# Performance work log

Measured on AMD Instinct MI355X. Metric: run time of the kernel, lower is better.

Reference implementation:

```python
import jax, jax.numpy as jnp
import numpy as np

MERSENNE_P = (1 << 31) - 1  # prime used by universal hashing


def _uhash_cols(random_numbers, n_full_cols, n_comp_cols):
    """Universal-hash map from full-weight column index -> compressed column index.
    h(j) = ((r0*j + r1) mod P) mod n_comp_cols  (ints stay well within int64).
    """
    j = jnp.arange(n_full_cols, dtype=jnp.int64)
    r0 = random_numbers[0]
    r1 = random_numbers[1]
    return ((r0 * j + r1) % MERSENNE_P) % n_comp_cols


def setup_inputs() -> dict:
    key = jax.random.key(0)
    k1, k2, k3 = jax.random.split(key, 3)
    in_features, out_features, redn_factor = 8192, 8192, 4
    init_scale = 1.0 / np.sqrt(in_features)
    x = jax.random.normal(k1, (64, in_features), dtype=jnp.float32)
    weight = jax.random.uniform(
        k2, (out_features, in_features // redn_factor), dtype=jnp.float32,
        minval=-init_scale, maxval=init_scale)
    random_numbers = jax.random.randint(k3, (4,), 1, 1048576, dtype=jnp.int64)
    return {"x": x, "weight": weight, "random_numbers": random_numbers,
            "redn_factor": 4}


def reference(x, weight, random_numbers, redn_factor):
    # x: [..., K]; weight (compressed): [N, K // redn_factor]
    orig_shape = x.shape
    K = orig_shape[-1]
    x2d = x.reshape(-1, K)                      # preprocess: flatten leading dims
    n_comp = weight.shape[1]
    col_idx = _uhash_cols(random_numbers, K, n_comp)   # [K] hashed gather indices
    w_full = weight[:, col_idx]                 # [N, K] expanded via hashed gather
    y = x2d @ w_full.T                          # [rows, N]
    return y.reshape(*orig_shape[:-1], y.shape[-1])  # postprocess
```

## Files before the change

### kernel.cpp

```cpp
#include <hip/hip_runtime.h>
#include <hip/hip_bf16.h>

#define K_FULL   8192
#define M_ROWS   64
#define N_OUT    8192
#define N_COMP   2048
#define P_MERS   2147483647


typedef __attribute__((ext_vector_type(8))) short bf16x8;
typedef __attribute__((ext_vector_type(4))) float f32x4;

__device__ __forceinline__ short f2bfs(float f) {
    __hip_bfloat16 h = __float2bfloat16(f);
    return *reinterpret_cast<short*>(&h);
}
__device__ __forceinline__ unsigned int pk2bf(float a, float b) {
    return (unsigned int)(unsigned short)f2bfs(a)
         | ((unsigned int)(unsigned short)f2bfs(b) << 16);
}

#define GLL(g, l) __builtin_amdgcn_global_load_lds(                          \
    (const __attribute__((address_space(1))) unsigned int*)(g),             \
    (__attribute__((address_space(3))) unsigned int*)(l), 16, 0, 0)

__device__ __forceinline__ int hash_col(int j, int rn0, int rn1, int rn2, int rn3) {
    if (rn1 == 0 && rn3 == 0) {
        unsigned long long xx = (unsigned long long)(unsigned int)rn0 * (unsigned int)j
                              + (unsigned long long)(unsigned int)rn2;
        unsigned long long t = (xx & (unsigned long long)P_MERS) + (xx >> 31);
        if (t >= (unsigned long long)P_MERS) t -= (unsigned long long)P_MERS;
        return (int)(t & (N_COMP - 1));
    } else {
        unsigned int t = (unsigned int)rn0 * (unsigned int)j + (unsigned int)rn1;
        int ti = (int)t;
        int m1 = ti % P_MERS;
        if (m1 < 0) m1 += P_MERS;
        return m1 & (N_COMP - 1);
    }
}

__global__ __launch_bounds__(1024) void k_xc(const float* __restrict__ x,
                                             const int* __restrict__ rn,
                                             unsigned int* __restrict__ xcF) {
    __shared__ float row[N_COMP];
    const int m = blockIdx.x;
    const int tid = threadIdx.x;
    row[tid] = 0.0f;
    row[tid + 1024] = 0.0f;
    const int rn0 = rn[0], rn1 = rn[1], rn2 = rn[2], rn3 = rn[3];
    __syncthreads();

    const float* xm = x + (size_t)m * K_FULL;
#pragma unroll
    for (int it = 0; it < 2; ++it) {
        int j0 = tid * 4 + it * 4096;
        float4 v = *(const float4*)(xm + j0);
        atomicAdd(&row[hash_col(j0 + 0, rn0, rn1, rn2, rn3)], v.x);
        atomicAdd(&row[hash_col(j0 + 1, rn0, rn1, rn2, rn3)], v.y);
        atomicAdd(&row[hash_col(j0 + 2, rn0, rn1, rn2, rn3)], v.z);
        atomicAdd(&row[hash_col(j0 + 3, rn0, rn1, rn2, rn3)], v.w);
    }
    __syncthreads();

    const int c0 = 2 * tid;
    const int s  = c0 >> 5;
    const int kg = (c0 >> 3) & 3;
    const int e0 = c0 & 7;
    const int g  = m >> 4;
    const int nr = m & 15;
    xcF[(((s * 4 + g) * 64 + kg * 16 + nr) << 2) + (e0 >> 1)] =
        pk2bf(row[c0], row[c0 + 1]);
}

#define WT_ROWD 260
#define WT_TILE (16 * WT_ROWD)

__global__ __launch_bounds__(512) void k_gemm(const float* __restrict__ W,
                                              const unsigned short* __restrict__ xcF,
                                              float* __restrict__ y) {
    __shared__ float wt[2][WT_TILE];
    __shared__ float ys[8][M_ROWS][16];
    const int tid  = threadIdx.x;
    const int lane = tid & 63;
    const int w    = __builtin_amdgcn_readfirstlane(tid >> 6);
    const int nr   = lane & 15;
    const int kg   = lane >> 4;
    const int n0   = blockIdx.x * 16;
    const int rot  = (blockIdx.x >> 3) & 7;
    const int r0   = 2 * w;

    const float* g0 = W + (size_t)(n0 + r0) * N_COMP + lane * 4;
    const float* g1 = g0 + N_COMP;
    const unsigned short* ab = xcF + (size_t)w * 2048 + lane * 8;

    f32x4 acc0 = {0.f, 0.f, 0.f, 0.f};
    f32x4 acc1 = {0.f, 0.f, 0.f, 0.f};
    f32x4 acc2 = {0.f, 0.f, 0.f, 0.f};
    f32x4 acc3 = {0.f, 0.f, 0.f, 0.f};

    GLL(g0 + rot * 256, &wt[0][r0 * WT_ROWD]);
    GLL(g1 + rot * 256, &wt[0][(r0 + 1) * WT_ROWD]);
    __syncthreads();

#pragma unroll 1
    for (int p = 0; p < 8; ++p) {
        const int b  = p & 1;
        const int pm = (p + rot) & 7;
        const int pn = (p + 1 + rot) & 7;
        if (p < 7) {
            GLL(g0 + pn * 256, &wt[b ^ 1][r0 * WT_ROWD]);
            GLL(g1 + pn * 256, &wt[b ^ 1][(r0 + 1) * WT_ROWD]);
        }
        const unsigned short* ap = ab + (size_t)pm * 16384;
        bf16x8 a0 = *(const bf16x8*)(ap);
        bf16x8 a1 = *(const bf16x8*)(ap + 512);
        bf16x8 a2 = *(const bf16x8*)(ap + 1024);
        bf16x8 a3 = *(const bf16x8*)(ap + 1536);
        const float* bp = &wt[b][nr * WT_ROWD + w * 32 + kg * 8];
        float4 f0 = *(const float4*)(bp);
        float4 f1 = *(const float4*)(bp + 4);
        bf16x8 bf;
        bf[0] = f2bfs(f0.x); bf[1] = f2bfs(f0.y);
        bf[2] = f2bfs(f0.z); bf[3] = f2bfs(f0.w);
        bf[4] = f2bfs(f1.x); bf[5] = f2bfs(f1.y);
        bf[6] = f2bfs(f1.z); bf[7] = f2bfs(f1.w);
        acc0 = __builtin_amdgcn_mfma_f32_16x16x32_bf16(a0, bf, acc0, 0, 0, 0);
        acc1 = __builtin_amdgcn_mfma_f32_16x16x32_bf16(a1, bf, acc1, 0, 0, 0);
        acc2 = __builtin_amdgcn_mfma_f32_16x16x32_bf16(a2, bf, acc2, 0, 0, 0);
        acc3 = __builtin_amdgcn_mfma_f32_16x16x32_bf16(a3, bf, acc3, 0, 0, 0);
        __syncthreads();
    }

#pragma unroll
    for (int j = 0; j < 4; ++j) {
        ys[w][ 0 + kg * 4 + j][nr] = acc0[j];
        ys[w][16 + kg * 4 + j][nr] = acc1[j];
        ys[w][32 + kg * 4 + j][nr] = acc2[j];
        ys[w][48 + kg * 4 + j][nr] = acc3[j];
    }
    __syncthreads();

#pragma unroll
    for (int i = 0; i < 2; ++i) {
        int o = tid + 512 * i;
        int m = o >> 4;
        int n = o & 15;
        float s = 0.f;
#pragma unroll
        for (int q = 0; q < 8; ++q) s += ys[q][m][n];
        y[(size_t)m * N_OUT + n0 + n] = s;
    }
}

extern "C" void kernel_launch(void* const* d_in, const int* in_sizes, int n_in,
                              void* d_out, int out_size, void* d_ws, size_t ws_size,
                              hipStream_t stream) {
    const float* x = (const float*)d_in[0];
    const float* W = (const float*)d_in[1];
    const int* rn  = (const int*)d_in[2];
    float* y       = (float*)d_out;

    unsigned int* xcF = (unsigned int*)d_ws;

    k_xc<<<M_ROWS, 1024, 0, stream>>>(x, rn, xcF);
    k_gemm<<<N_OUT / 16, 512, 0, stream>>>(W, (const unsigned short*)xcF, y);
}
```

Baseline: 30.76 us.

## Fuse hashed x compression and GEMM into one cooperative kernel with grid sync

Merges the x-compression kernel and the GEMM kernel into a single cooperative launch. The first 64 blocks build the hashed compressed rows in LDS (reusing the ys buffer) and write them to workspace, a grid-wide sync follows, and then every block runs the GEMM. The first W tile prefetch is issued before the compression so it overlaps that phase. This removes a kernel launch boundary at the cost of a grid barrier. It also requires all 512 blocks to be co-resident, which is why launch bounds now request 4 blocks per CU.

```diff
diff --git a/kernel.cpp b/kernel.cpp
--- a/kernel.cpp
+++ b/kernel.cpp
@@ -1,5 +1,8 @@
 #include <hip/hip_runtime.h>
 #include <hip/hip_bf16.h>
+#include <hip/hip_cooperative_groups.h>
+
+namespace cg = cooperative_groups;
 
 #define K_FULL   8192
 #define M_ROWS   64
@@ -40,68 +43,73 @@
     }
 }
 
-__global__ __launch_bounds__(1024) void k_xc(const float* __restrict__ x,
-                                             const int* __restrict__ rn,
-                                             unsigned int* __restrict__ xcF) {
-    __shared__ float row[N_COMP];
-    const int m = blockIdx.x;
-    const int tid = threadIdx.x;
-    row[tid] = 0.0f;
-    row[tid + 1024] = 0.0f;
-    const int rn0 = rn[0], rn1 = rn[1], rn2 = rn[2], rn3 = rn[3];
-    __syncthreads();
-
-    const float* xm = x + (size_t)m * K_FULL;
-#pragma unroll
-    for (int it = 0; it < 2; ++it) {
-        int j0 = tid * 4 + it * 4096;
-        float4 v = *(const float4*)(xm + j0);
-        atomicAdd(&row[hash_col(j0 + 0, rn0, rn1, rn2, rn3)], v.x);
-        atomicAdd(&row[hash_col(j0 + 1, rn0, rn1, rn2, rn3)], v.y);
-        atomicAdd(&row[hash_col(j0 + 2, rn0, rn1, rn2, rn3)], v.z);
-        atomicAdd(&row[hash_col(j0 + 3, rn0, rn1, rn2, rn3)], v.w);
-    }
-    __syncthreads();
-
-    const int c0 = 2 * tid;
-    const int s  = c0 >> 5;
-    const int kg = (c0 >> 3) & 3;
-    const int e0 = c0 & 7;
-    const int g  = m >> 4;
-    const int nr = m & 15;
-    xcF[(((s * 4 + g) * 64 + kg * 16 + nr) << 2) + (e0 >> 1)] =
-        pk2bf(row[c0], row[c0 + 1]);
-}
-
 #define WT_ROWD 260
 #define WT_TILE (16 * WT_ROWD)
 
-__global__ __launch_bounds__(512) void k_gemm(const float* __restrict__ W,
-                                              const unsigned short* __restrict__ xcF,
-                                              float* __restrict__ y) {
+__global__ __launch_bounds__(512, 4) void k_fused(const float* __restrict__ x,
+                                                  const float* __restrict__ W,
+                                                  const int* __restrict__ rn,
+                                                  unsigned int* __restrict__ xcFu,
+                                                  float* __restrict__ y) {
     __shared__ float wt[2][WT_TILE];
     __shared__ float ys[8][M_ROWS][16];
+    float* row = &ys[0][0][0];
+
     const int tid  = threadIdx.x;
     const int lane = tid & 63;
     const int w    = __builtin_amdgcn_readfirstlane(tid >> 6);
     const int nr   = lane & 15;
     const int kg   = lane >> 4;
-    const int n0   = blockIdx.x * 16;
-    const int rot  = (blockIdx.x >> 3) & 7;
+    const int bid  = blockIdx.x;
+    const int n0   = bid * 16;
+    const int rot  = (bid >> 3) & 7;
     const int r0   = 2 * w;
 
     const float* g0 = W + (size_t)(n0 + r0) * N_COMP + lane * 4;
     const float* g1 = g0 + N_COMP;
-    const unsigned short* ab = xcF + (size_t)w * 2048 + lane * 8;
 
+    GLL(g0 + rot * 256, &wt[0][r0 * WT_ROWD]);
+    GLL(g1 + rot * 256, &wt[0][(r0 + 1) * WT_ROWD]);
+
+    if (bid < M_ROWS) {
+        const int m = bid;
+        row[tid] = 0.f; row[tid + 512] = 0.f;
+        row[tid + 1024] = 0.f; row[tid + 1536] = 0.f;
+        const int rn0 = rn[0], rn1 = rn[1], rn2 = rn[2], rn3 = rn[3];
+        __syncthreads();
+        const float* xm = x + (size_t)m * K_FULL;
+#pragma unroll
+        for (int it = 0; it < 4; ++it) {
+            int j0 = tid * 4 + it * 2048;
+            float4 v = *(const float4*)(xm + j0);
+            atomicAdd(&row[hash_col(j0 + 0, rn0, rn1, rn2, rn3)], v.x);
+            atomicAdd(&row[hash_col(j0 + 1, rn0, rn1, rn2, rn3)], v.y);
+            atomicAdd(&row[hash_col(j0 + 2, rn0, rn1, rn2, rn3)], v.z);
+            atomicAdd(&row[hash_col(j0 + 3, rn0, rn1, rn2, rn3)], v.w);
+        }
+        __syncthreads();
+        const int g  = m >> 4;
+        const int mr = m & 15;
+#pragma unroll
+        for (int q = 0; q < 2; ++q) {
+            const int c0 = 2 * (tid + q * 512);
+            const int s  = c0 >> 5;
+            const int kq = (c0 >> 3) & 3;
+            const int e0 = c0 & 7;
+            xcFu[(((s * 4 + g) * 64 + kq * 16 + mr) << 2) + (e0 >> 1)] =
+                pk2bf(row[c0], row[c0 + 1]);
+        }
+        __threadfence();
+    }
+
+    cg::this_grid().sync();
+
+    const unsigned short* ab = (const unsigned short*)xcFu
+                             + (size_t)w * 2048 + lane * 8;
     f32x4 acc0 = {0.f, 0.f, 0.f, 0.f};
     f32x4 acc1 = {0.f, 0.f, 0.f, 0.f};
     f32x4 acc2 = {0.f, 0.f, 0.f, 0.f};
     f32x4 acc3 = {0.f, 0.f, 0.f, 0.f};
-
-    GLL(g0 + rot * 256, &wt[0][r0 * WT_ROWD]);
-    GLL(g1 + rot * 256, &wt[0][(r0 + 1) * WT_ROWD]);
-    __syncthreads();
 
 #pragma unroll 1
     for (int p = 0; p < 8; ++p) {
@@ -160,9 +168,9 @@
     const float* W = (const float*)d_in[1];
     const int* rn  = (const int*)d_in[2];
     float* y       = (float*)d_out;
-
     unsigned int* xcF = (unsigned int*)d_ws;
 
-    k_xc<<<M_ROWS, 1024, 0, stream>>>(x, rn, xcF);
-    k_gemm<<<N_OUT / 16, 512, 0, stream>>>(W, (const unsigned short*)xcF, y);
+    void* args[] = { (void*)&x, (void*)&W, (void*)&rn, (void*)&xcF, (void*)&y };
+    hipLaunchCooperativeKernel((const void*)k_fused, dim3(N_OUT / 16), dim3(512),
+                               args, 0, stream);
 }
```

New measurement: 101.6 us. 230% more time.
